# Optimization experiments

Measured on AMD Instinct MI355X. Metric: run time of the kernel, lower is better.

Reference implementation:

```python
import jax, jax.numpy as jnp
import numpy as np

B, L, H, E, V, Z, T = 256, 2, 1024, 256, 28, 1024, 512
SOS_IDX, EOS_IDX = 1, 0


def setup_inputs() -> dict:
    key = jax.random.key(0)
    ks = jax.random.split(key, 16)
    s = 0.05
    emb = s * jax.random.normal(ks[0], (V, E), jnp.float32)
    emb = emb.at[EOS_IDX].set(0.0)  # padding_idx=0
    return {
        "z": jax.random.normal(ks[1], (B, Z), jnp.float32),
        "emb": emb,
        "w_zh": s * jax.random.normal(ks[2], (L * H, Z), jnp.float32),
        "b_zh": jnp.zeros((L * H,), jnp.float32),
        "w_ih0": s * jax.random.normal(ks[3], (3 * H, E), jnp.float32),
        "w_hh0": s * jax.random.normal(ks[4], (3 * H, H), jnp.float32),
        "b_ih0": jnp.zeros((3 * H,), jnp.float32),
        "b_hh0": jnp.zeros((3 * H,), jnp.float32),
        "w_ih1": s * jax.random.normal(ks[5], (3 * H, H), jnp.float32),
        "w_hh1": s * jax.random.normal(ks[6], (3 * H, H), jnp.float32),
        "b_ih1": jnp.zeros((3 * H,), jnp.float32),
        "b_hh1": jnp.zeros((3 * H,), jnp.float32),
        "w_out": s * jax.random.normal(ks[7], (V, H), jnp.float32),
        "b_out": jnp.zeros((V,), jnp.float32),
    }


def _gru_cell(x, h, w_ih, w_hh, b_ih, b_hh):
    # PyTorch GRU cell math
    gi = x @ w_ih.T + b_ih          # [B, 3H]
    gh = h @ w_hh.T + b_hh          # [B, 3H]
    i_r, i_z, i_n = jnp.split(gi, 3, axis=-1)
    h_r, h_z, h_n = jnp.split(gh, 3, axis=-1)
    r = jax.nn.sigmoid(i_r + h_r)
    zg = jax.nn.sigmoid(i_z + h_z)
    n = jnp.tanh(i_n + r * h_n)
    return (1.0 - zg) * n + zg * h


def reference(z, emb, w_zh, b_zh, w_ih0, w_hh0, b_ih0, b_hh0,
              w_ih1, w_hh1, b_ih1, b_hh1, w_out, b_out):
    # init hidden from latent: (B, L*H) -> per-layer (B, H)
    h = jnp.tanh(z @ w_zh.T + b_zh).reshape(-1, L, H)
    h0, h1 = h[:, 0, :], h[:, 1, :]
    tok0 = jnp.full((z.shape[0],), SOS_IDX, jnp.int32)
    keys = jax.random.split(jax.random.key(42), T)

    def step(carry, k):
        tok, h0, h1 = carry
        x = emb[tok]                         # [B, E] embedding lookup
        h0n = _gru_cell(x, h0, w_ih0, w_hh0, b_ih0, b_hh0)
        h1n = _gru_cell(h0n, h1, w_ih1, w_hh1, b_ih1, b_hh1)
        logit = h1n @ w_out.T + b_out        # [B, V]
        tok_n = jax.random.categorical(k, logit)  # multinomial(softmax(logit))
        return (tok_n, h0n, h1n), (logit, tok_n)

    _, (logits, tokens) = jax.lax.scan(step, (tok0, h0, h1), keys)
    # [T, B, V] -> [B, T, V]; [T, B] -> [B, T]
    return logits.transpose(1, 0, 2), tokens.T
```

## Files before the change

kernel.cpp:

```cpp
#include <hip/hip_runtime.h>

#define BB 256
#define HH 1024
#define EE 256
#define VV 28
#define ZZ 1024
#define TT 512
#define G3 3072
#define NTHR 256
#define TOKBASE (BB * TT * VV)

#define BM 64
#define BN 64
#define KT 32

#define MMN 48
#define NBN 64

typedef float f4 __attribute__((ext_vector_type(4)));
typedef float f32x4 __attribute__((ext_vector_type(4)));
typedef _Float16 f16x8 __attribute__((ext_vector_type(8)));
typedef unsigned short u16x4 __attribute__((ext_vector_type(4)));
typedef unsigned short u16x8 __attribute__((ext_vector_type(8)));

#define RES_SCALE 512.0f
#define INV_RES (1.0f / 512.0f)

__device__ __align__(16) float g_h0[2][BB][HH];
__device__ __align__(16) float g_h1[2][BB][HH];
__device__ __align__(16) float g_gh0b[BB][G3];
__device__ __align__(16) float g_gh1b[BB][G3];
__device__ __align__(16) float g_gi1[BB][G3];
__device__ __align__(16) float g_P0[VV][G3];
__device__ __align__(16) unsigned short g_h0t[32][2][4][BB][8];
__device__ __align__(16) unsigned short g_h1t[32][2][4][BB][8];
__device__ __align__(16) unsigned short g_wt[3][NBN][32][2][4][MMN][8];

__device__ __forceinline__ uint2 tf2x32(unsigned k0, unsigned k1,
                                        unsigned x0, unsigned x1) {
  unsigned ks2 = k0 ^ k1 ^ 0x1BD11BDAu;
  unsigned ksl[3] = {k0, k1, ks2};
  x0 += k0; x1 += k1;
#pragma unroll
  for (int g = 0; g < 5; ++g) {
    const int r0 = (g & 1) ? 17 : 13;
    const int r1 = (g & 1) ? 29 : 15;
    const int r2 = (g & 1) ? 16 : 26;
    const int r3 = (g & 1) ? 24 : 6;
    x0 += x1; x1 = (x1 << r0) | (x1 >> (32 - r0)); x1 ^= x0;
    x0 += x1; x1 = (x1 << r1) | (x1 >> (32 - r1)); x1 ^= x0;
    x0 += x1; x1 = (x1 << r2) | (x1 >> (32 - r2)); x1 ^= x0;
    x0 += x1; x1 = (x1 << r3) | (x1 >> (32 - r3)); x1 ^= x0;
    x0 += ksl[(g + 1) % 3];
    x1 += ksl[(g + 2) % 3] + (unsigned)(g + 1);
  }
  return make_uint2(x0, x1);
}

__device__ __forceinline__ float sigf(float x) {
  return 1.0f / (1.0f + expf(-x));
}

__device__ __forceinline__ float gru_h(float i_r, float h_r, float i_z, float h_z,
                                       float i_n, float h_n, float hprev) {
  float r  = sigf(i_r + h_r);
  float zg = sigf(i_z + h_z);
  float n  = tanhf(i_n + r * h_n);
  return (1.0f - zg) * n + zg * hprev;
}

__device__ __forceinline__ void split2(float x, unsigned short& a,
                                       unsigned short& b) {
  _Float16 h1 = (_Float16)x;
  _Float16 h2 = (_Float16)((x - (float)h1) * RES_SCALE);
  a = __builtin_bit_cast(unsigned short, h1);
  b = __builtin_bit_cast(unsigned short, h2);
}

__device__ __forceinline__ void gload16(unsigned short* l, const unsigned short* g) {
  __builtin_amdgcn_global_load_lds(
      (const __attribute__((address_space(1))) unsigned int*)(g),
      (__attribute__((address_space(3))) unsigned int*)(l), 16, 0, 0);
}

__device__ __forceinline__ void gemm_unit(
    const float* __restrict__ At, int lda, int rows_valid,
    const float* __restrict__ Wt, int ldw,
    const float* __restrict__ bias,
    float* __restrict__ Ct, int ldc,
    int K, int mode,
    float (&As)[BM][KT + 4], float (&Ws)[KT][BN + 4]) {
  const int tid = threadIdx.x;
  const int tx = tid & 15, ty = tid >> 4;
  f4 acc0 = {0.f, 0.f, 0.f, 0.f};
  f4 acc1 = {0.f, 0.f, 0.f, 0.f};
  f4 acc2 = {0.f, 0.f, 0.f, 0.f};
  f4 acc3 = {0.f, 0.f, 0.f, 0.f};

  for (int kb = 0; kb < K; kb += KT) {
#pragma unroll
    for (int l = 0; l < 2; ++l) {
      int f = tid + l * NTHR;
      int r = f >> 3, kq = (f & 7) << 2;
      f4 v = {0.f, 0.f, 0.f, 0.f};
      if (r < rows_valid) v = *(const f4*)(At + r * lda + kb + kq);
      *(f4*)&As[r][kq] = v;
    }
#pragma unroll
    for (int l = 0; l < 2; ++l) {
      int f = tid + l * NTHR;
      int nr = f >> 3, kq = (f & 7) << 2;
      f4 v = *(const f4*)(Wt + nr * ldw + kb + kq);
      Ws[kq + 0][nr] = v[0];
      Ws[kq + 1][nr] = v[1];
      Ws[kq + 2][nr] = v[2];
      Ws[kq + 3][nr] = v[3];
    }
    __syncthreads();
#pragma unroll
    for (int kk = 0; kk < KT; kk += 4) {
      f4 a0 = *(const f4*)&As[(ty << 2) + 0][kk];
      f4 a1 = *(const f4*)&As[(ty << 2) + 1][kk];
      f4 a2 = *(const f4*)&As[(ty << 2) + 2][kk];
      f4 a3 = *(const f4*)&As[(ty << 2) + 3][kk];
      f4 b0 = *(const f4*)&Ws[kk + 0][tx << 2];
      f4 b1 = *(const f4*)&Ws[kk + 1][tx << 2];
      f4 b2 = *(const f4*)&Ws[kk + 2][tx << 2];
      f4 b3 = *(const f4*)&Ws[kk + 3][tx << 2];
      acc0 += b0 * a0[0]; acc0 += b1 * a0[1]; acc0 += b2 * a0[2]; acc0 += b3 * a0[3];
      acc1 += b0 * a1[0]; acc1 += b1 * a1[1]; acc1 += b2 * a1[2]; acc1 += b3 * a1[3];
      acc2 += b0 * a2[0]; acc2 += b1 * a2[1]; acc2 += b2 * a2[2]; acc2 += b3 * a2[3];
      acc3 += b0 * a3[0]; acc3 += b1 * a3[1]; acc3 += b2 * a3[2]; acc3 += b3 * a3[3];
    }
    __syncthreads();
  }

  f4 accs[4] = {acc0, acc1, acc2, acc3};
#pragma unroll
  for (int i = 0; i < 4; ++i) {
    int r = (ty << 2) + i;
    if (r < rows_valid) {
#pragma unroll
      for (int j = 0; j < 4; ++j) {
        int c = (tx << 2) + j;
        float v = accs[i][j] + bias[c];
        if (mode == 1) v = tanhf(v);
        Ct[r * ldc + c] = v;
      }
    }
  }
}

#define A_CH (2 * 4 * 128)
#define W_CH (2 * 4 * MMN)
#define BUFSZ ((A_CH + W_CH) * 8)

__device__ __forceinline__ void mm_tile(
    const unsigned short* __restrict__ At,
    const unsigned short* __restrict__ Wt,
    const float* __restrict__ bias,
    float* __restrict__ C,
    int m0, int n0, unsigned short* lds) {
  const int tid = threadIdx.x;
  const int wr = tid >> 6, lane = tid & 63;
  const int lr = lane & 15, lk8 = lane >> 4;
  const bool hiW = (tid < 128);

  f32x4 acc1[2][3] = {};
  f32x4 accR[2][3] = {};

  auto stage = [&](unsigned short* lbuf, int ks) {
    unsigned short* lA = lbuf;
    unsigned short* lW = lbuf + A_CH * 8;
    const unsigned short* abase = At + (size_t)ks * (2 * 4 * BB * 8);
#pragma unroll
    for (int r = 0; r < 4; ++r) {
      int j = r * NTHR + tid;
      int skk = j >> 7, row = j & 127;
      gload16(lA + j * 8, abase + ((size_t)skk * BB + m0 + row) * 8);
    }
    const unsigned short* wbase = Wt + (size_t)ks * (W_CH * 8);
    gload16(lW + tid * 8, wbase + (size_t)tid * 8);
    if (tid < W_CH - NTHR) {
      int j = NTHR + tid;
      gload16(lW + j * 8, wbase + (size_t)j * 8);
    }
  };

  auto compute = [&](const unsigned short* lbuf) {
    const unsigned short* lA = lbuf;
    const unsigned short* lW = lbuf + A_CH * 8;
    f16x8 a[2][2], b[3][2];
#pragma unroll
    for (int mi = 0; mi < 2; ++mi)
#pragma unroll
      for (int s = 0; s < 2; ++s)
        a[mi][s] = *(const f16x8*)(lA + (((s << 2) | lk8) * 128 + wr * 32 + mi * 16 + lr) * 8);
#pragma unroll
    for (int ni = 0; ni < 3; ++ni)
#pragma unroll
      for (int s = 0; s < 2; ++s)
        b[ni][s] = *(const f16x8*)(lW + (((s << 2) | lk8) * MMN + ni * 16 + lr) * 8);
    __builtin_amdgcn_s_setprio(1);
#pragma unroll
    for (int mi = 0; mi < 2; ++mi)
#pragma unroll
      for (int ni = 0; ni < 3; ++ni) {
        acc1[mi][ni] = __builtin_amdgcn_mfma_f32_16x16x32_f16(a[mi][0], b[ni][0], acc1[mi][ni], 0, 0, 0);
        accR[mi][ni] = __builtin_amdgcn_mfma_f32_16x16x32_f16(a[mi][0], b[ni][1], accR[mi][ni], 0, 0, 0);
        accR[mi][ni] = __builtin_amdgcn_mfma_f32_16x16x32_f16(a[mi][1], b[ni][0], accR[mi][ni], 0, 0, 0);
      }
    __builtin_amdgcn_s_setprio(0);
  };

  stage(lds, 0);
  stage(lds + BUFSZ, 1);
  for (int ks = 0; ks < 32; ++ks) {
    if (ks < 31) {
      if (hiW) asm volatile("s_waitcnt vmcnt(6)" ::: "memory");
      else     asm volatile("s_waitcnt vmcnt(5)" ::: "memory");
    } else {
      asm volatile("s_waitcnt vmcnt(0)" ::: "memory");
    }
    __builtin_amdgcn_s_barrier();
    compute(lds + (ks % 3) * BUFSZ);
    if (ks + 2 < 32) stage(lds + ((ks + 2) % 3) * BUFSZ, ks + 2);
  }

#pragma unroll
  for (int mi = 0; mi < 2; ++mi) {
    int rowb = m0 + wr * 32 + mi * 16 + ((lane >> 4) << 2);
#pragma unroll
    for (int ni = 0; ni < 3; ++ni) {
      int col = n0 + ni * 16 + lr;
      float bv = bias[col];
#pragma unroll
      for (int r = 0; r < 4; ++r)
        C[(size_t)(rowb + r) * G3 + col] = acc1[mi][ni][r] + accR[mi][ni][r] * INV_RES + bv;
    }
  }
}

__device__ __forceinline__ void write_ht(unsigned short (*ht)[2][4][BB][8],
                                         int row, int k0,
                                         u16x4 o1, u16x4 o2) {
  const int ks = k0 >> 5, kk = (k0 >> 3) & 3, e0 = k0 & 7;
  *(u16x4*)&ht[ks][0][kk][row][e0] = o1;
  *(u16x4*)&ht[ks][1][kk][row][e0] = o2;
}

__global__ __launch_bounds__(NTHR) void k_setup1(
    const float* __restrict__ z, const float* __restrict__ w_zh,
    const float* __restrict__ b_zh, const float* __restrict__ emb,
    const float* __restrict__ w_ih0, const float* __restrict__ b_ih0) {
  __shared__ __align__(16) float As[BM][KT + 4];
  __shared__ __align__(16) float Ws[KT][BN + 4];
  const int bid = blockIdx.x;
  if (bid < 128) {
    int m0 = (bid >> 5) * BM;
    int n0 = (bid & 31) * BN;
    float* Cb;
    int col;
    if (n0 < HH) { Cb = &g_h0[1][0][0]; col = n0; }
    else         { Cb = &g_h1[1][0][0]; col = n0 - HH; }
    gemm_unit(z + m0 * ZZ, ZZ, BM, w_zh + n0 * ZZ, ZZ, b_zh + n0,
              Cb + m0 * HH + col, HH, ZZ, 1, As, Ws);
  } else {
    int n0 = (bid - 128) * BN;
    gemm_unit(emb, EE, VV, w_ih0 + n0 * EE, EE, b_ih0 + n0,
              &g_P0[0][0] + n0, G3, EE, 0, As, Ws);
  }
}

__global__ __launch_bounds__(NTHR) void k_splitw(
    const float* __restrict__ w_ih1, const float* __restrict__ w_hh0,
    const float* __restrict__ w_hh1) {
  unsigned u = blockIdx.x * NTHR + threadIdx.x;
  int row = u % MMN;
  unsigned v = u / MMN;
  int kk = v & 3, ks = (v >> 2) & 31;
  unsigned rem = v >> 7;
  int mat = rem / NBN, bn = rem % NBN;
  const float* src = (mat == 0) ? w_ih1 : (mat == 1) ? w_hh0 : w_hh1;
  const float* p = src + (size_t)(bn * MMN + row) * HH + ks * 32 + kk * 8;
  f4 v0 = *(const f4*)p;
  f4 v1 = *(const f4*)(p + 4);
  u16x8 o1, o2;
#pragma unroll
  for (int c = 0; c < 8; ++c) {
    float x = (c < 4) ? v0[c] : v1[c - 4];
    unsigned short a, b;
    split2(x, a, b);
    o1[c] = a; o2[c] = b;
  }
  *(u16x8*)&g_wt[mat][bn][ks][0][kk][row][0] = o1;
  *(u16x8*)&g_wt[mat][bn][ks][1][kk][row][0] = o2;
}

__global__ __launch_bounds__(NTHR) void k_splith() {
  unsigned e = blockIdx.x * NTHR + threadIdx.x;
  int mat = e >> 16, r = (e >> 8) & 255, k0 = (e & 255) << 2;
  const float* src = (mat == 0) ? &g_h0[1][0][0] : &g_h1[1][0][0];
  f4 v = *(const f4*)(src + (size_t)r * HH + k0);
  u16x4 o1, o2;
#pragma unroll
  for (int c = 0; c < 4; ++c) {
    unsigned short a, b;
    split2(v[c], a, b);
    o1[c] = a; o2[c] = b;
  }
  write_ht((mat == 0) ? g_h0t : g_h1t, r, k0, o1, o2);
}

__global__ __launch_bounds__(NTHR, 2) void k_mm_init(const float* __restrict__ b_hh0) {
  __shared__ __align__(16) unsigned short lds[3 * BUFSZ];
  int mt = blockIdx.x >> 6, bn = blockIdx.x & 63;
  mm_tile(&g_h0t[0][0][0][0][0], &g_wt[1][bn][0][0][0][0][0], b_hh0,
          &g_gh0b[0][0], mt * 128, bn * MMN, lds);
}

__global__ __launch_bounds__(NTHR) void k_gate0_init() {
  const int b = blockIdx.x, tid = threadIdx.x, j = tid << 2;
  const float* __restrict__ gi = g_P0[1];
  const float* __restrict__ gh = g_gh0b[b];
  f4 ir = *(const f4*)&gi[j];
  f4 iz = *(const f4*)&gi[j + HH];
  f4 in_ = *(const f4*)&gi[j + 2 * HH];
  f4 hr = *(const f4*)&gh[j];
  f4 hz = *(const f4*)&gh[j + HH];
  f4 hn = *(const f4*)&gh[j + 2 * HH];
  f4 hp = *(const f4*)&g_h0[1][b][j];
  f4 ho;
  u16x4 o1, o2;
#pragma unroll
  for (int c = 0; c < 4; ++c) {
    ho[c] = gru_h(ir[c], hr[c], iz[c], hz[c], in_[c], hn[c], hp[c]);
    unsigned short a, bb2;
    split2(ho[c], a, bb2);
    o1[c] = a; o2[c] = bb2;
  }
  *(f4*)&g_h0[0][b][j] = ho;
  write_ht(g_h0t, b, j, o1, o2);
}

__global__ __launch_bounds__(NTHR, 2) void k_mm(
    const float* __restrict__ b_ih1, const float* __restrict__ b_hh0,
    const float* __restrict__ b_hh1) {
  __shared__ __align__(16) unsigned short lds[3 * BUFSZ];
  const int bid = blockIdx.x;
  const int mt = bid / 192, r = bid % 192;
  const int mat = r >> 6, bn = r & 63;
  const unsigned short* At = (mat == 2) ? &g_h1t[0][0][0][0][0] : &g_h0t[0][0][0][0][0];
  const unsigned short* Wt = &g_wt[mat][bn][0][0][0][0][0];
  const float* bias = (mat == 0) ? b_ih1 : (mat == 1) ? b_hh0 : b_hh1;
  float* C = (mat == 0) ? &g_gi1[0][0] : (mat == 1) ? &g_gh0b[0][0] : &g_gh1b[0][0];
  mm_tile(At, Wt, bias, C, mt * 128, bn * MMN, lds);
}

__global__ __launch_bounds__(NTHR) void k_fuse(
    int t, const float* __restrict__ w_out, const float* __restrict__ b_out,
    float* __restrict__ out) {
  __shared__ __align__(16) float s_h[HH];
  __shared__ float s_log[32];
  __shared__ float s_score[32];
  __shared__ int s_tok;
  const int b = blockIdx.x, tid = threadIdx.x, j = tid << 2;
  const int pw = t & 1, pr = pw ^ 1;

  {
    const float* __restrict__ gi = g_gi1[b];
    const float* __restrict__ gh = g_gh1b[b];
    f4 ir = *(const f4*)&gi[j];
    f4 iz = *(const f4*)&gi[j + HH];
    f4 in_ = *(const f4*)&gi[j + 2 * HH];
    f4 hr = *(const f4*)&gh[j];
    f4 hz = *(const f4*)&gh[j + HH];
    f4 hn = *(const f4*)&gh[j + 2 * HH];
    f4 hp = *(const f4*)&g_h1[pr][b][j];
    f4 ho;
    u16x4 o1, o2;
#pragma unroll
    for (int c = 0; c < 4; ++c) {
      ho[c] = gru_h(ir[c], hr[c], iz[c], hz[c], in_[c], hn[c], hp[c]);
      unsigned short a, bb2;
      split2(ho[c], a, bb2);
      o1[c] = a; o2[c] = bb2;
    }
    *(f4*)&g_h1[pw][b][j] = ho;
    *(f4*)&s_h[j] = ho;
    write_ht(g_h1t, b, j, o1, o2);
  }
  __syncthreads();

  {
    const int v = tid >> 3, ks = tid & 7;
    float part = 0.f;
    if (v < VV) {
      const float* __restrict__ wrow = w_out + v * HH + ks * 128;
      const float* __restrict__ hh = s_h + ks * 128;
#pragma unroll 8
      for (int i = 0; i < 128; i += 4) {
        f4 wv = *(const f4*)&wrow[i];
        f4 hv = *(const f4*)&hh[i];
        part += hv[0] * wv[0] + hv[1] * wv[1] + hv[2] * wv[2] + hv[3] * wv[3];
      }
    }
    part += __shfl_xor(part, 1);
    part += __shfl_xor(part, 2);
    part += __shfl_xor(part, 4);
    if (v < VV && ks == 0) s_log[v] = part;
  }
  __syncthreads();

  if (tid < VV) {
    float logit = s_log[tid] + b_out[tid];
    out[(size_t)b * (TT * VV) + (size_t)t * VV + tid] = logit;
    uint2 kt = tf2x32(0u, 42u, 0u, (unsigned)t);
    uint2 rr = tf2x32(kt.x, kt.y, 0u, (unsigned)(b * VV + tid));
    unsigned bits = rr.x ^ rr.y;
    float uf = __uint_as_float((bits >> 9) | 0x3f800000u) - 1.0f;
    if (uf <= 0.0f) uf = 1.17549435e-38f;
    s_score[tid] = logit - logf(-logf(uf));
  }
  __syncthreads();
  if (tid == 0) {
    float best = s_score[0];
    int bv = 0;
    for (int vv = 1; vv < VV; ++vv) {
      float s = s_score[vv];
      if (s > best) { best = s; bv = vv; }
    }
    s_tok = bv;
    out[TOKBASE + (size_t)b * TT + t] = (float)bv;
  }
  __syncthreads();

  {
    const int tok = s_tok;
    const float* __restrict__ gi = g_P0[tok];
    const float* __restrict__ gh = g_gh0b[b];
    f4 ir = *(const f4*)&gi[j];
    f4 iz = *(const f4*)&gi[j + HH];
    f4 in_ = *(const f4*)&gi[j + 2 * HH];
    f4 hr = *(const f4*)&gh[j];
    f4 hz = *(const f4*)&gh[j + HH];
    f4 hn = *(const f4*)&gh[j + 2 * HH];
    f4 hp = *(const f4*)&g_h0[pw][b][j];
    f4 ho;
    u16x4 o1, o2;
#pragma unroll
    for (int c = 0; c < 4; ++c) {
      ho[c] = gru_h(ir[c], hr[c], iz[c], hz[c], in_[c], hn[c], hp[c]);
      unsigned short a, bb2;
      split2(ho[c], a, bb2);
      o1[c] = a; o2[c] = bb2;
    }
    *(f4*)&g_h0[pr][b][j] = ho;
    write_ht(g_h0t, b, j, o1, o2);
  }
}

extern "C" void kernel_launch(void* const* d_in, const int* in_sizes, int n_in,
                              void* d_out, int out_size, void* d_ws, size_t ws_size,
                              hipStream_t stream) {
  (void)in_sizes; (void)n_in; (void)d_ws; (void)ws_size; (void)out_size;
  const float* z     = (const float*)d_in[0];
  const float* emb   = (const float*)d_in[1];
  const float* w_zh  = (const float*)d_in[2];
  const float* b_zh  = (const float*)d_in[3];
  const float* w_ih0 = (const float*)d_in[4];
  const float* w_hh0 = (const float*)d_in[5];
  const float* b_ih0 = (const float*)d_in[6];
  const float* b_hh0 = (const float*)d_in[7];
  const float* w_ih1 = (const float*)d_in[8];
  const float* w_hh1 = (const float*)d_in[9];
  const float* b_ih1 = (const float*)d_in[10];
  const float* b_hh1 = (const float*)d_in[11];
  const float* w_out = (const float*)d_in[12];
  const float* b_out = (const float*)d_in[13];
  float* out = (float*)d_out;

  k_setup1<<<dim3(176), dim3(NTHR), 0, stream>>>(z, w_zh, b_zh, emb, w_ih0, b_ih0);
  k_splitw<<<dim3(4608), dim3(NTHR), 0, stream>>>(w_ih1, w_hh0, w_hh1);
  k_splith<<<dim3(512), dim3(NTHR), 0, stream>>>();
  k_mm_init<<<dim3(128), dim3(NTHR), 0, stream>>>(b_hh0);
  k_gate0_init<<<dim3(BB), dim3(NTHR), 0, stream>>>();

  for (int t = 0; t < TT; ++t) {
    k_mm<<<dim3(384), dim3(NTHR), 0, stream>>>(b_ih1, b_hh0, b_hh1);
    k_fuse<<<dim3(BB), dim3(NTHR), 0, stream>>>(t, w_out, b_out, out);
  }
}
```

Baseline: 15.96 ms.

## Load GEMM A fragments directly into registers, keep only weights in LDS

The mm_tile GEMM no longer stages the activation (A) tile through shared memory. Each wave now loads its own A fragments from global memory straight into registers, using a three-deep register ring buffer. Only the weight tile still goes through a triple-buffered LDS pipeline, and the main loop is unrolled by three so the rotating buffers can be named statically. This is meant to cut LDS traffic and footprint and the LDS read latency on A, at the cost of more VGPR pressure and reliance on hand-written vmcnt counts that must still match the new load mix.

Measured after the change: 16.15 ms. About the same (+1.2%).

```diff
diff --git a/kernel.cpp b/kernel.cpp
--- a/kernel.cpp
+++ b/kernel.cpp
@@ -151,9 +151,9 @@
   }
 }
 
-#define A_CH (2 * 4 * 128)
 #define W_CH (2 * 4 * MMN)
-#define BUFSZ ((A_CH + W_CH) * 8)
+#define WBUF (W_CH * 8)
+#define A_KS_STRIDE (2 * 4 * BB * 8)
 
 __device__ __forceinline__ void mm_tile(
     const unsigned short* __restrict__ At,
@@ -169,17 +169,19 @@
   f32x4 acc1[2][3] = {};
   f32x4 accR[2][3] = {};
 
-  auto stage = [&](unsigned short* lbuf, int ks) {
-    unsigned short* lA = lbuf;
-    unsigned short* lW = lbuf + A_CH * 8;
-    const unsigned short* abase = At + (size_t)ks * (2 * 4 * BB * 8);
-#pragma unroll
-    for (int r = 0; r < 4; ++r) {
-      int j = r * NTHR + tid;
-      int skk = j >> 7, row = j & 127;
-      gload16(lA + j * 8, abase + ((size_t)skk * BB + m0 + row) * 8);
-    }
-    const unsigned short* wbase = Wt + (size_t)ks * (W_CH * 8);
+  const unsigned short* afrag = At + ((size_t)lk8 * BB + m0 + wr * 32 + lr) * 8;
+
+  auto loadA = [&](int ks, f16x8 (&a)[2][2]) {
+    const unsigned short* p = afrag + (size_t)ks * A_KS_STRIDE;
+#pragma unroll
+    for (int mi = 0; mi < 2; ++mi)
+#pragma unroll
+      for (int s = 0; s < 2; ++s)
+        a[mi][s] = *(const f16x8*)(p + (size_t)s * (4 * BB * 8) + mi * 128);
+  };
+
+  auto stageW = [&](unsigned short* lW, int ks) {
+    const unsigned short* wbase = Wt + (size_t)ks * WBUF;
     gload16(lW + tid * 8, wbase + (size_t)tid * 8);
     if (tid < W_CH - NTHR) {
       int j = NTHR + tid;
@@ -187,15 +189,8 @@
     }
   };
 
-  auto compute = [&](const unsigned short* lbuf) {
-    const unsigned short* lA = lbuf;
-    const unsigned short* lW = lbuf + A_CH * 8;
-    f16x8 a[2][2], b[3][2];
-#pragma unroll
-    for (int mi = 0; mi < 2; ++mi)
-#pragma unroll
-      for (int s = 0; s < 2; ++s)
-        a[mi][s] = *(const f16x8*)(lA + (((s << 2) | lk8) * 128 + wr * 32 + mi * 16 + lr) * 8);
+  auto compute = [&](const unsigned short* lW, f16x8 (&a)[2][2]) {
+    f16x8 b[3][2];
 #pragma unroll
     for (int ni = 0; ni < 3; ++ni)
 #pragma unroll
@@ -213,19 +208,36 @@
     __builtin_amdgcn_s_setprio(0);
   };
 
-  stage(lds, 0);
-  stage(lds + BUFSZ, 1);
-  for (int ks = 0; ks < 32; ++ks) {
-    if (ks < 31) {
-      if (hiW) asm volatile("s_waitcnt vmcnt(6)" ::: "memory");
-      else     asm volatile("s_waitcnt vmcnt(5)" ::: "memory");
-    } else {
-      asm volatile("s_waitcnt vmcnt(0)" ::: "memory");
-    }
-    __builtin_amdgcn_s_barrier();
-    compute(lds + (ks % 3) * BUFSZ);
-    if (ks + 2 < 32) stage(lds + ((ks + 2) % 3) * BUFSZ, ks + 2);
-  }
+  f16x8 A0[2][2], A1[2][2], A2[2][2];
+  unsigned short* W0 = lds;
+  unsigned short* W1 = lds + WBUF;
+  unsigned short* W2 = lds + 2 * WBUF;
+
+  stageW(W0, 0); loadA(0, A0);
+  stageW(W1, 1); loadA(1, A1);
+
+#define PHASE(ks, Ac, Wc, Ap, Wp)                                   \
+  do {                                                              \
+    if (hiW) asm volatile("s_waitcnt vmcnt(6)" ::: "memory");       \
+    else     asm volatile("s_waitcnt vmcnt(5)" ::: "memory");       \
+    __builtin_amdgcn_s_barrier();                                   \
+    loadA((ks) + 2, Ap); stageW(Wp, (ks) + 2);                      \
+    compute(Wc, Ac);                                                \
+  } while (0)
+
+  for (int kb = 0; kb < 30; kb += 3) {
+    PHASE(kb + 0, A0, W0, A2, W2);
+    PHASE(kb + 1, A1, W1, A0, W0);
+    PHASE(kb + 2, A2, W2, A1, W1);
+  }
+#undef PHASE
+  if (hiW) asm volatile("s_waitcnt vmcnt(6)" ::: "memory");
+  else     asm volatile("s_waitcnt vmcnt(5)" ::: "memory");
+  __builtin_amdgcn_s_barrier();
+  compute(W0, A0);
+  asm volatile("s_waitcnt vmcnt(0)" ::: "memory");
+  __builtin_amdgcn_s_barrier();
+  compute(W1, A1);
 
 #pragma unroll
   for (int mi = 0; mi < 2; ++mi) {
@@ -313,7 +325,7 @@
 }
 
 __global__ __launch_bounds__(NTHR, 2) void k_mm_init(const float* __restrict__ b_hh0) {
-  __shared__ __align__(16) unsigned short lds[3 * BUFSZ];
+  __shared__ __align__(16) unsigned short lds[3 * WBUF];
   int mt = blockIdx.x >> 6, bn = blockIdx.x & 63;
   mm_tile(&g_h0t[0][0][0][0][0], &g_wt[1][bn][0][0][0][0][0], b_hh0,
           &g_gh0b[0][0], mt * 128, bn * MMN, lds);
@@ -346,7 +358,7 @@
 __global__ __launch_bounds__(NTHR, 2) void k_mm(
     const float* __restrict__ b_ih1, const float* __restrict__ b_hh0,
     const float* __restrict__ b_hh1) {
-  __shared__ __align__(16) unsigned short lds[3 * BUFSZ];
+  __shared__ __align__(16) unsigned short lds[3 * WBUF];
   const int bid = blockIdx.x;
   const int mt = bid / 192, r = bid % 192;
   const int mat = r >> 6, bn = r & 63;
```

## Cover the full batch per matmul block with 512 threads and prefetch earlier

Applied to the files above, without the earlier changes.

The per-step GRU matmul kernel now gives each block all 256 batch rows using 8 waves, instead of 128 rows with 4 waves. Each weight slice is therefore staged into LDS once rather than twice, and the grid shrinks from 384 to 192 blocks. The next stage's global-to-LDS loads are now issued right after the barrier, before compute, and the wait counts are adjusted to match. The cost is that each block needs about 114KB of LDS, so probably only one block fits per CU, and fewer blocks than CUs are launched, which may reduce parallelism and latency hiding.

After: 17.57 ms. 1.1x slower.

```diff
diff --git a/kernel.cpp b/kernel.cpp
--- a/kernel.cpp
+++ b/kernel.cpp
@@ -16,6 +16,7 @@
 
 #define MMN 48
 #define NBN 64
+#define MMTHR 512
 
 typedef float f4 __attribute__((ext_vector_type(4)));
 typedef float f32x4 __attribute__((ext_vector_type(4)));
@@ -151,7 +152,7 @@
   }
 }
 
-#define A_CH (2 * 4 * 128)
+#define A_CH (2 * 4 * 256)
 #define W_CH (2 * 4 * MMN)
 #define BUFSZ ((A_CH + W_CH) * 8)
 
@@ -160,11 +161,11 @@
     const unsigned short* __restrict__ Wt,
     const float* __restrict__ bias,
     float* __restrict__ C,
-    int m0, int n0, unsigned short* lds) {
+    int n0, unsigned short* lds) {
   const int tid = threadIdx.x;
-  const int wr = tid >> 6, lane = tid & 63;
+  const int w = tid >> 6, lane = tid & 63;
   const int lr = lane & 15, lk8 = lane >> 4;
-  const bool hiW = (tid < 128);
+  const bool hiW = (tid < W_CH);
 
   f32x4 acc1[2][3] = {};
   f32x4 accR[2][3] = {};
@@ -172,19 +173,14 @@
   auto stage = [&](unsigned short* lbuf, int ks) {
     unsigned short* lA = lbuf;
     unsigned short* lW = lbuf + A_CH * 8;
-    const unsigned short* abase = At + (size_t)ks * (2 * 4 * BB * 8);
+    const unsigned short* abase = At + (size_t)ks * (A_CH * 8);
 #pragma unroll
     for (int r = 0; r < 4; ++r) {
-      int j = r * NTHR + tid;
-      int skk = j >> 7, row = j & 127;
-      gload16(lA + j * 8, abase + ((size_t)skk * BB + m0 + row) * 8);
+      int j = r * MMTHR + tid;
+      gload16(lA + j * 8, abase + (size_t)j * 8);
     }
     const unsigned short* wbase = Wt + (size_t)ks * (W_CH * 8);
-    gload16(lW + tid * 8, wbase + (size_t)tid * 8);
-    if (tid < W_CH - NTHR) {
-      int j = NTHR + tid;
-      gload16(lW + j * 8, wbase + (size_t)j * 8);
-    }
+    if (tid < W_CH) gload16(lW + tid * 8, wbase + (size_t)tid * 8);
   };
 
   auto compute = [&](const unsigned short* lbuf) {
@@ -195,7 +191,7 @@
     for (int mi = 0; mi < 2; ++mi)
 #pragma unroll
       for (int s = 0; s < 2; ++s)
-        a[mi][s] = *(const f16x8*)(lA + (((s << 2) | lk8) * 128 + wr * 32 + mi * 16 + lr) * 8);
+        a[mi][s] = *(const f16x8*)(lA + (((s << 2) | lk8) * 256 + w * 32 + mi * 16 + lr) * 8);
 #pragma unroll
     for (int ni = 0; ni < 3; ++ni)
 #pragma unroll
@@ -217,19 +213,19 @@
   stage(lds + BUFSZ, 1);
   for (int ks = 0; ks < 32; ++ks) {
     if (ks < 31) {
-      if (hiW) asm volatile("s_waitcnt vmcnt(6)" ::: "memory");
-      else     asm volatile("s_waitcnt vmcnt(5)" ::: "memory");
+      if (hiW) asm volatile("s_waitcnt vmcnt(5)" ::: "memory");
+      else     asm volatile("s_waitcnt vmcnt(4)" ::: "memory");
     } else {
       asm volatile("s_waitcnt vmcnt(0)" ::: "memory");
     }
     __builtin_amdgcn_s_barrier();
+    if (ks + 2 < 32) stage(lds + ((ks + 2) % 3) * BUFSZ, ks + 2);
     compute(lds + (ks % 3) * BUFSZ);
-    if (ks + 2 < 32) stage(lds + ((ks + 2) % 3) * BUFSZ, ks + 2);
   }
 
 #pragma unroll
   for (int mi = 0; mi < 2; ++mi) {
-    int rowb = m0 + wr * 32 + mi * 16 + ((lane >> 4) << 2);
+    int rowb = w * 32 + mi * 16 + ((lane >> 4) << 2);
 #pragma unroll
     for (int ni = 0; ni < 3; ++ni) {
       int col = n0 + ni * 16 + lr;
@@ -312,11 +308,11 @@
   write_ht((mat == 0) ? g_h0t : g_h1t, r, k0, o1, o2);
 }
 
-__global__ __launch_bounds__(NTHR, 2) void k_mm_init(const float* __restrict__ b_hh0) {
+__global__ __launch_bounds__(MMTHR, 2) void k_mm_init(const float* __restrict__ b_hh0) {
   __shared__ __align__(16) unsigned short lds[3 * BUFSZ];
-  int mt = blockIdx.x >> 6, bn = blockIdx.x & 63;
+  int bn = blockIdx.x;
   mm_tile(&g_h0t[0][0][0][0][0], &g_wt[1][bn][0][0][0][0][0], b_hh0,
-          &g_gh0b[0][0], mt * 128, bn * MMN, lds);
+          &g_gh0b[0][0], bn * MMN, lds);
 }
 
 __global__ __launch_bounds__(NTHR) void k_gate0_init() {
@@ -343,18 +339,17 @@
   write_ht(g_h0t, b, j, o1, o2);
 }
 
-__global__ __launch_bounds__(NTHR, 2) void k_mm(
+__global__ __launch_bounds__(MMTHR, 2) void k_mm(
     const float* __restrict__ b_ih1, const float* __restrict__ b_hh0,
     const float* __restrict__ b_hh1) {
   __shared__ __align__(16) unsigned short lds[3 * BUFSZ];
   const int bid = blockIdx.x;
-  const int mt = bid / 192, r = bid % 192;
-  const int mat = r >> 6, bn = r & 63;
+  const int mat = bid >> 6, bn = bid & 63;
   const unsigned short* At = (mat == 2) ? &g_h1t[0][0][0][0][0] : &g_h0t[0][0][0][0][0];
   const unsigned short* Wt = &g_wt[mat][bn][0][0][0][0][0];
   const float* bias = (mat == 0) ? b_ih1 : (mat == 1) ? b_hh0 : b_hh1;
   float* C = (mat == 0) ? &g_gi1[0][0] : (mat == 1) ? &g_gh0b[0][0] : &g_gh1b[0][0];
-  mm_tile(At, Wt, bias, C, mt * 128, bn * MMN, lds);
+  mm_tile(At, Wt, bias, C, bn * MMN, lds);
 }
 
 __global__ __launch_bounds__(NTHR) void k_fuse(
@@ -483,11 +478,11 @@
   k_setup1<<<dim3(176), dim3(NTHR), 0, stream>>>(z, w_zh, b_zh, emb, w_ih0, b_ih0);
   k_splitw<<<dim3(4608), dim3(NTHR), 0, stream>>>(w_ih1, w_hh0, w_hh1);
   k_splith<<<dim3(512), dim3(NTHR), 0, stream>>>();
-  k_mm_init<<<dim3(128), dim3(NTHR), 0, stream>>>(b_hh0);
+  k_mm_init<<<dim3(64), dim3(MMTHR), 0, stream>>>(b_hh0);
   k_gate0_init<<<dim3(BB), dim3(NTHR), 0, stream>>>();
 
   for (int t = 0; t < TT; ++t) {
-    k_mm<<<dim3(384), dim3(NTHR), 0, stream>>>(b_ih1, b_hh0, b_hh1);
+    k_mm<<<dim3(192), dim3(MMTHR), 0, stream>>>(b_ih1, b_hh0, b_hh1);
     k_fuse<<<dim3(BB), dim3(NTHR), 0, stream>>>(t, w_out, b_out, out);
   }
 }
```
